# Kernel tuning notes

Measured on AMD Instinct MI355X. Metric: run time of the kernel, lower is better.

The kernel has to match this reference:

```python
import jax, jax.numpy as jnp
import numpy as np

OUT_H, OUT_W = 7, 7
SCALE = 0.25
S = 2  # sample_num per bin axis


def _bilinear(img, y, x):
    """Bilinearly sample img[..., H, W] at float coords (y, x).
    y, x have identical shape G; returns img.shape[:-2] + G.
    Matches RoIAlign CUDA interpolation (zero outside [-1, H]/[-1, W])."""
    H, W = img.shape[-2], img.shape[-1]
    valid = (y > -1.0) & (y < H) & (x > -1.0) & (x < W)
    y = jnp.clip(y, 0.0, H - 1)
    x = jnp.clip(x, 0.0, W - 1)
    y0 = jnp.floor(y).astype(jnp.int32)
    x0 = jnp.floor(x).astype(jnp.int32)
    y1 = jnp.minimum(y0 + 1, H - 1)
    x1 = jnp.minimum(x0 + 1, W - 1)
    ly = y - y0
    lx = x - x0
    hy, hx = 1.0 - ly, 1.0 - lx
    v = (hy * hx * img[..., y0, x0] + hy * lx * img[..., y0, x1]
         + ly * hx * img[..., y1, x0] + ly * lx * img[..., y1, x1])
    return jnp.where(valid, v, 0.0)


def setup_inputs() -> dict:
    key = jax.random.key(0)
    k1, k2, k3, k4, k5 = jax.random.split(key, 5)
    N, C, H, W = 2, 256, 200, 200
    R, MH, MW = 512, 128, 128
    features = jax.random.normal(k1, (N, C, H, W), jnp.float32)
    bidx = jax.random.randint(k2, (R,), 0, N)
    xy1 = jax.random.randint(k3, (R, 2), 0, 672)          # x1, y1 (image coords)
    wh = jax.random.randint(k4, (R, 2), 8, 128)           # box sizes in [8,128)
    xy2 = jnp.minimum(xy1 + wh - 1, 799)                  # x2, y2 inclusive
    rois = jnp.concatenate([bidx[:, None].astype(jnp.float32),
                            xy1.astype(jnp.float32),
                            xy2.astype(jnp.float32)], axis=1)  # [R,5]
    batch_masks = jax.random.uniform(k5, (R, MH, MW), jnp.float32)
    # zero-pad beyond each roi's (h, w), mimicking the list->dense packing
    hv = jnp.arange(MH)[None, :] < (xy2[:, 1] - xy1[:, 1] + 1)[:, None]
    wv = jnp.arange(MW)[None, :] < (xy2[:, 0] - xy1[:, 0] + 1)[:, None]
    batch_masks = batch_masks * (hv[:, :, None] & wv[:, None, :]).astype(jnp.float32)
    return {"features": features, "rois": rois, "batch_masks": batch_masks}


def reference(features, rois, batch_masks):
    """Mask-weighted RoIAlign: per-roi bilinear feature samples are weighted by
    the roi's shape mask (bilinearly sampled in roi-relative image coords),
    then average-pooled over the sub-sample grid of each output bin."""
    C = features.shape[1]

    def one_roi(roi, mask):
        b = roi[0].astype(jnp.int32)
        x1, y1, x2, y2 = roi[1], roi[2], roi[3], roi[4]
        roi_start_w = x1 * SCALE
        roi_start_h = y1 * SCALE
        roi_w = jnp.maximum((x2 - x1 + 1.0) * SCALE, 1.0)
        roi_h = jnp.maximum((y2 - y1 + 1.0) * SCALE, 1.0)
        bin_w = roi_w / OUT_W
        bin_h = roi_h / OUT_H
        # sub-sample offsets: (bin + (i+0.5)/S) for i in [0,S)  -> [OUT*S]
        offs = (jnp.arange(S, dtype=jnp.float32) + 0.5) / S
        ys = roi_start_h + (jnp.arange(OUT_H, dtype=jnp.float32)[:, None] + offs[None, :]).reshape(-1) * bin_h
        xs = roi_start_w + (jnp.arange(OUT_W, dtype=jnp.float32)[:, None] + offs[None, :]).reshape(-1) * bin_w
        yy, xx = jnp.meshgrid(ys, xs, indexing='ij')       # [OUT_H*S, OUT_W*S]
        feat = features[b]                                  # [C, H, W]
        vals = _bilinear(feat, yy, xx)                      # [C, OUT_H*S, OUT_W*S]
        # mask weight at the same sample point, in roi-relative image coords
        my = jnp.clip(yy / SCALE - y1, 0.0, y2 - y1)
        mx = jnp.clip(xx / SCALE - x1, 0.0, x2 - x1)
        wgt = _bilinear(mask, my, mx)                       # [OUT_H*S, OUT_W*S]
        v = (vals * wgt).reshape(C, OUT_H, S, OUT_W, S)
        return v.mean(axis=(2, 4))                          # [C, OUT_H, OUT_W]

    return jax.vmap(one_roi)(rois, batch_masks)             # [R, C, OUT_H, OUT_W]
```

## Files before the change

### kernel.cpp

```cpp
#include <hip/hip_runtime.h>


constexpr int   OUT_H = 7, OUT_W = 7;
constexpr int   NBIN  = OUT_H * OUT_W;
constexpr float SCALE = 0.25f;
constexpr int   S     = 2;
constexpr int   NSAMP = NBIN * S * S;
constexpr int   CG    = 8;
constexpr int   NPAIR = CG / 2;
constexpr int   RDIM  = 34;
constexpr int   RCOLS = 40;
constexpr int   NPIX  = RDIM * RCOLS;
constexpr int   PSTRIDE = NPIX * 2 + 4;

typedef unsigned short ushort_t;

__device__ __forceinline__ ushort_t f2bf(float f) {
    unsigned u = __float_as_uint(f);
    u += 0x7fffu + ((u >> 16) & 1u);
    return (ushort_t)(u >> 16);
}

__global__ __launch_bounds__(256, 6)
void roialign_direct_kernel(const float* __restrict__ features,
                            const float* __restrict__ rois,
                            const float* __restrict__ masks,
                            float*       __restrict__ out,
                            int C, int H, int W, int MH, int MW) {
    __shared__ __align__(16) ushort_t s_reg[NPAIR * PSTRIDE];
    __shared__ ushort4 s_idx[NSAMP];
    __shared__ float4  s_w[NSAMP];

    const int r   = blockIdx.x;
    const int cg  = blockIdx.y;
    const int tid = threadIdx.x;

    const float* roi = rois + (size_t)r * 5;
    const int   b  = (int)roi[0];
    const float x1 = roi[1], y1 = roi[2], x2 = roi[3], y2 = roi[4];

    const float roi_start_w = x1 * SCALE;
    const float roi_start_h = y1 * SCALE;
    const float roi_w = fmaxf((x2 - x1 + 1.0f) * SCALE, 1.0f);
    const float roi_h = fmaxf((y2 - y1 + 1.0f) * SCALE, 1.0f);
    const float bin_w = roi_w * (1.0f / OUT_W);
    const float bin_h = roi_h * (1.0f / OUT_H);

    int y_lo = (int)floorf(roi_start_h); y_lo = max(0, min(y_lo, H - 1));
    int x_lo = (int)floorf(roi_start_w); x_lo = max(0, min(x_lo, W - 1));
    const int y_hi = max(y_lo, min((int)floorf(roi_start_h + roi_h) + 1, H - 1));
    const int x_hi = max(x_lo, min((int)floorf(roi_start_w + roi_w) + 1, W - 1));
    const int rows  = min(y_hi - y_lo + 1, RDIM);
    const int x_lo4 = x_lo & ~3;
    const int cols4 = min((x_hi - x_lo4 + 4) >> 2, RCOLS / 4);

    {
        const int g    = tid >> 5;
        const int lane = tid & 31;
        const int pr   = g >> 1;
        const int part = g & 1;
        const size_t HWs = (size_t)H * W;
        const float* srcE = features + ((size_t)b * C + (size_t)(cg * CG + 2 * pr)) * HWs
                          + (size_t)y_lo * W + x_lo4;
        const float* srcO = srcE + HWs;
        unsigned* dp32base = (unsigned*)(s_reg + pr * PSTRIDE);
        const int items = rows * cols4;
        const float rcp = 1.0f / (float)cols4;
        for (int it = lane + part * 32; it < items; it += 64) {
            int ry = (int)((float)it * rcp);
            int k  = it - ry * cols4;
            if (k >= cols4) { ry++; k -= cols4; }
            if (k < 0)      { ry--; k += cols4; }
            const float4 vE = *(const float4*)(srcE + ry * W + 4 * k);
            const float4 vO = *(const float4*)(srcO + ry * W + 4 * k);
            const int pix = ry * RCOLS + 4 * k;
            uint2 a, c2;
            a.x  = (unsigned)f2bf(vE.x) | ((unsigned)f2bf(vO.x) << 16);
            a.y  = (unsigned)f2bf(vE.y) | ((unsigned)f2bf(vO.y) << 16);
            c2.x = (unsigned)f2bf(vE.z) | ((unsigned)f2bf(vO.z) << 16);
            c2.y = (unsigned)f2bf(vE.w) | ((unsigned)f2bf(vO.w) << 16);
            *(uint2*)(dp32base + pix)     = a;
            *(uint2*)(dp32base + pix + 2) = c2;
        }
    }

    if (tid < NSAMP) {
        const int bin = tid >> 2;
        const int sub = tid & 3;
        const int ph  = bin / OUT_W, pw = bin % OUT_W;
        const int iy  = sub >> 1,   ix = sub & 1;

        const float yy = roi_start_h + ((float)ph + ((float)iy + 0.5f) * (1.0f / S)) * bin_h;
        const float xx = roi_start_w + ((float)pw + ((float)ix + 0.5f) * (1.0f / S)) * bin_w;

        const bool valid = (yy > -1.0f) && (yy < (float)H) && (xx > -1.0f) && (xx < (float)W);

        const float* msk = masks + (size_t)r * MH * MW;
        float my = fminf(fmaxf(yy * (1.0f / SCALE) - y1, 0.0f), y2 - y1);
        float mx = fminf(fmaxf(xx * (1.0f / SCALE) - x1, 0.0f), x2 - x1);
        my = fminf(fmaxf(my, 0.0f), (float)(MH - 1));
        mx = fminf(fmaxf(mx, 0.0f), (float)(MW - 1));
        const int my0 = (int)floorf(my), mx0 = (int)floorf(mx);
        const int my1 = min(my0 + 1, MH - 1), mx1 = min(mx0 + 1, MW - 1);
        const float mly = my - (float)my0, mlx = mx - (float)mx0;
        const float mhy = 1.0f - mly,      mhx = 1.0f - mlx;
        const float wgt = mhy * mhx * msk[my0 * MW + mx0] + mhy * mlx * msk[my0 * MW + mx1]
                        + mly * mhx * msk[my1 * MW + mx0] + mly * mlx * msk[my1 * MW + mx1];

        const float yc = fminf(fmaxf(yy, 0.0f), (float)(H - 1));
        const float xc = fminf(fmaxf(xx, 0.0f), (float)(W - 1));
        const int y0  = (int)floorf(yc), x0 = (int)floorf(xc);
        const int y1i = min(y0 + 1, H - 1), x1i = min(x0 + 1, W - 1);
        const float ly = yc - (float)y0, lx = xc - (float)x0;
        const float hy = 1.0f - ly,      hx = 1.0f - lx;

        const int ly0 = min(max(y0  - y_lo,  0), RDIM  - 1);
        const int ly1 = min(max(y1i - y_lo,  0), RDIM  - 1);
        const int lx0 = min(max(x0  - x_lo4, 0), RCOLS - 1);
        const int lx1 = min(max(x1i - x_lo4, 0), RCOLS - 1);

        const float scale_all = (valid ? wgt : 0.0f) * (1.0f / (float)(S * S));
        ushort4 ix4;
        ix4.x = (ushort_t)((ly0 * RCOLS + lx0) * 4);
        ix4.y = (ushort_t)((ly0 * RCOLS + lx1) * 4);
        ix4.z = (ushort_t)((ly1 * RCOLS + lx0) * 4);
        ix4.w = (ushort_t)((ly1 * RCOLS + lx1) * 4);
        s_idx[tid] = ix4;
        float4 w4;
        w4.x = hy * hx * scale_all;
        w4.y = hy * lx * scale_all;
        w4.z = ly * hx * scale_all;
        w4.w = ly * lx * scale_all;
        s_w[tid] = w4;
    }
    __syncthreads();

    float accE = 0.0f, accO = 0.0f;
    const int pr  = tid & 3;
    const int bin = tid >> 2;
    if (tid < NSAMP) {
        const char* base = (const char*)s_reg + pr * (PSTRIDE * 2);
#pragma unroll
        for (int sub = 0; sub < 4; ++sub) {
            const int s = bin * 4 + sub;
            const ushort4 off = s_idx[s];
            const float4  w   = s_w[s];
            const unsigned q0 = *(const unsigned*)(base + off.x);
            const unsigned q1 = *(const unsigned*)(base + off.y);
            const unsigned q2 = *(const unsigned*)(base + off.z);
            const unsigned q3 = *(const unsigned*)(base + off.w);
            accE = fmaf(w.x, __uint_as_float(q0 << 16),          accE);
            accO = fmaf(w.x, __uint_as_float(q0 & 0xffff0000u),  accO);
            accE = fmaf(w.y, __uint_as_float(q1 << 16),          accE);
            accO = fmaf(w.y, __uint_as_float(q1 & 0xffff0000u),  accO);
            accE = fmaf(w.z, __uint_as_float(q2 << 16),          accE);
            accO = fmaf(w.z, __uint_as_float(q2 & 0xffff0000u),  accO);
            accE = fmaf(w.w, __uint_as_float(q3 << 16),          accE);
            accO = fmaf(w.w, __uint_as_float(q3 & 0xffff0000u),  accO);
        }
    }
    __syncthreads();

    float* s_out = (float*)s_reg;
    if (tid < NSAMP) {
        s_out[(2 * pr + 0) * NBIN + bin] = accE;
        s_out[(2 * pr + 1) * NBIN + bin] = accO;
    }
    __syncthreads();

    float* outr = out + ((size_t)r * C + (size_t)cg * CG) * NBIN;
    for (int i = tid; i < CG * NBIN; i += 256)
        outr[i] = s_out[i];
}

__global__ __launch_bounds__(256)
void mask_roialign_kernel(const float* __restrict__ features,
                          const float* __restrict__ rois,
                          const float* __restrict__ masks,
                          float*       __restrict__ out,
                          int C, int H, int W, int MH, int MW) {
    int blk = blockIdx.x;
    int pw  = blk % OUT_W;
    int ph  = (blk / OUT_W) % OUT_H;
    int r   = blk / (OUT_W * OUT_H);
    int c   = threadIdx.x;
    if (c >= C) return;

    const float* roi = rois + (size_t)r * 5;
    int   b  = (int)roi[0];
    float x1 = roi[1], y1 = roi[2], x2 = roi[3], y2 = roi[4];

    float roi_start_w = x1 * SCALE;
    float roi_start_h = y1 * SCALE;
    float roi_w = fmaxf((x2 - x1 + 1.0f) * SCALE, 1.0f);
    float roi_h = fmaxf((y2 - y1 + 1.0f) * SCALE, 1.0f);
    float bin_w = roi_w / (float)OUT_W;
    float bin_h = roi_h / (float)OUT_H;

    const float* fch = features + ((size_t)b * C + c) * (size_t)(H * W);
    const float* msk = masks + (size_t)r * MH * MW;

    float acc = 0.0f;
#pragma unroll
    for (int iy = 0; iy < S; ++iy) {
        float yy = roi_start_h + ((float)ph + ((float)iy + 0.5f) / (float)S) * bin_h;
#pragma unroll
        for (int ix = 0; ix < S; ++ix) {
            float xx = roi_start_w + ((float)pw + ((float)ix + 0.5f) / (float)S) * bin_w;
            bool valid = (yy > -1.0f) && (yy < (float)H) && (xx > -1.0f) && (xx < (float)W);
            float my = fminf(fmaxf(yy / SCALE - y1, 0.0f), fminf(y2 - y1, (float)(MH - 1)));
            float mx = fminf(fmaxf(xx / SCALE - x1, 0.0f), fminf(x2 - x1, (float)(MW - 1)));
            int my0 = (int)floorf(my), mx0 = (int)floorf(mx);
            int my1 = min(my0 + 1, MH - 1), mx1 = min(mx0 + 1, MW - 1);
            float mly = my - my0, mlx = mx - mx0, mhy = 1.0f - mly, mhx = 1.0f - mlx;
            float wgt = mhy * mhx * msk[my0 * MW + mx0] + mhy * mlx * msk[my0 * MW + mx1]
                      + mly * mhx * msk[my1 * MW + mx0] + mly * mlx * msk[my1 * MW + mx1];
            if (valid) {
                float yc = fminf(fmaxf(yy, 0.0f), (float)(H - 1));
                float xc = fminf(fmaxf(xx, 0.0f), (float)(W - 1));
                int y0 = (int)floorf(yc), x0 = (int)floorf(xc);
                int y1i = min(y0 + 1, H - 1), x1i = min(x0 + 1, W - 1);
                float ly = yc - y0, lx = xc - x0, hy = 1.0f - ly, hx = 1.0f - lx;
                float v = hy * hx * fch[y0  * W + x0 ] + hy * lx * fch[y0  * W + x1i]
                        + ly * hx * fch[y1i * W + x0 ] + ly * lx * fch[y1i * W + x1i];
                acc += wgt * v;
            }
        }
    }
    out[((size_t)r * C + c) * (size_t)NBIN + ph * OUT_W + pw] = acc * (1.0f / (S * S));
}

extern "C" void kernel_launch(void* const* d_in, const int* in_sizes, int n_in,
                              void* d_out, int out_size, void* d_ws, size_t ws_size,
                              hipStream_t stream) {
    const float* features = (const float*)d_in[0];
    const float* rois     = (const float*)d_in[1];
    const float* masks    = (const float*)d_in[2];
    float*       out      = (float*)d_out;

    const int R  = in_sizes[1] / 5;
    const int C  = out_size / (R * NBIN);
    const int H  = 200, W = 200;
    const int MH = 128, MW = 128;

    (void)d_ws; (void)ws_size;

    if ((C % CG == 0) && (W % 4 == 0)) {
        roialign_direct_kernel<<<dim3(R, C / CG), dim3(256), 0, stream>>>(
            features, rois, masks, out, C, H, W, MH, MW);
    } else {
        mask_roialign_kernel<<<dim3(R * NBIN), dim3(256), 0, stream>>>(
            features, rois, masks, out, C, H, W, MH, MW);
    }
}
```

Before: 179.1 us.

## Swap grid order to group ROIs, hoist mask loads, use bf16 pair conversion

Swaps the grid so consecutive blocks share one ROI and walk over channel groups instead of walking over ROIs for a fixed channel group, which changes L2 reuse of the ROI's feature window and mask rows. Mask gathers are issued before the feature staging loop so their latency overlaps with it. The hand-written bf16 rounding is replaced with the library float2-to-bfloat162 conversion, and the staging loop is unrolled by two. Consecutive blocks now read different channel planes of the same spatial region, so L2 locality could get better or worse.

```diff
diff --git a/kernel.cpp b/kernel.cpp
--- a/kernel.cpp
+++ b/kernel.cpp
@@ -1,4 +1,5 @@
 #include <hip/hip_runtime.h>
+#include <hip/hip_bf16.h>
 
 
 constexpr int   OUT_H = 7, OUT_W = 7;
@@ -10,15 +11,15 @@
 constexpr int   NPAIR = CG / 2;
 constexpr int   RDIM  = 34;
 constexpr int   RCOLS = 40;
-constexpr int   NPIX  = RDIM * RCOLS;
-constexpr int   PSTRIDE = NPIX * 2 + 4;
+constexpr int   PSTRIDE = RDIM * RCOLS * 2 + 4;
 
 typedef unsigned short ushort_t;
 
-__device__ __forceinline__ ushort_t f2bf(float f) {
-    unsigned u = __float_as_uint(f);
-    u += 0x7fffu + ((u >> 16) & 1u);
-    return (ushort_t)(u >> 16);
+__device__ __forceinline__ unsigned pack_bf16_pair(float e, float o) {
+    __hip_bfloat162 h2 = __float22bfloat162_rn(make_float2(e, o));
+    unsigned u;
+    __builtin_memcpy(&u, &h2, sizeof(u));
+    return u;
 }
 
 __global__ __launch_bounds__(256, 6)
@@ -31,8 +32,8 @@
     __shared__ ushort4 s_idx[NSAMP];
     __shared__ float4  s_w[NSAMP];
 
-    const int r   = blockIdx.x;
-    const int cg  = blockIdx.y;
+    const int cgp = blockIdx.x;
+    const int r   = blockIdx.y;
     const int tid = threadIdx.x;
 
     const float* roi = rois + (size_t)r * 5;
@@ -54,18 +55,43 @@
     const int x_lo4 = x_lo & ~3;
     const int cols4 = min((x_hi - x_lo4 + 4) >> 2, RCOLS / 4);
 
+    float yy = 0.f, xx = 0.f, m00 = 0.f, m01 = 0.f, m10 = 0.f, m11 = 0.f;
+    float mly = 0.f, mlx = 0.f;
+    if (tid < NSAMP) {
+        const int bin = tid >> 2;
+        const int sub = tid & 3;
+        const int ph  = bin / OUT_W, pw = bin % OUT_W;
+        const int iy  = sub >> 1,   ix = sub & 1;
+        yy = roi_start_h + ((float)ph + ((float)iy + 0.5f) * (1.0f / S)) * bin_h;
+        xx = roi_start_w + ((float)pw + ((float)ix + 0.5f) * (1.0f / S)) * bin_w;
+
+        const float* msk = masks + (size_t)r * MH * MW;
+        float my = fminf(fmaxf(yy * (1.0f / SCALE) - y1, 0.0f), y2 - y1);
+        float mx = fminf(fmaxf(xx * (1.0f / SCALE) - x1, 0.0f), x2 - x1);
+        my = fminf(fmaxf(my, 0.0f), (float)(MH - 1));
+        mx = fminf(fmaxf(mx, 0.0f), (float)(MW - 1));
+        const int my0 = (int)floorf(my), mx0 = (int)floorf(mx);
+        const int my1 = min(my0 + 1, MH - 1), mx1 = min(mx0 + 1, MW - 1);
+        mly = my - (float)my0; mlx = mx - (float)mx0;
+        m00 = msk[my0 * MW + mx0];
+        m01 = msk[my0 * MW + mx1];
+        m10 = msk[my1 * MW + mx0];
+        m11 = msk[my1 * MW + mx1];
+    }
+
     {
         const int g    = tid >> 5;
         const int lane = tid & 31;
         const int pr   = g >> 1;
         const int part = g & 1;
         const size_t HWs = (size_t)H * W;
-        const float* srcE = features + ((size_t)b * C + (size_t)(cg * CG + 2 * pr)) * HWs
+        const float* srcE = features + ((size_t)b * C + (size_t)(cgp * CG + 2 * pr)) * HWs
                           + (size_t)y_lo * W + x_lo4;
         const float* srcO = srcE + HWs;
         unsigned* dp32base = (unsigned*)(s_reg + pr * PSTRIDE);
         const int items = rows * cols4;
         const float rcp = 1.0f / (float)cols4;
+#pragma unroll 2
         for (int it = lane + part * 32; it < items; it += 64) {
             int ry = (int)((float)it * rcp);
             int k  = it - ry * cols4;
@@ -75,37 +101,20 @@
             const float4 vO = *(const float4*)(srcO + ry * W + 4 * k);
             const int pix = ry * RCOLS + 4 * k;
             uint2 a, c2;
-            a.x  = (unsigned)f2bf(vE.x) | ((unsigned)f2bf(vO.x) << 16);
-            a.y  = (unsigned)f2bf(vE.y) | ((unsigned)f2bf(vO.y) << 16);
-            c2.x = (unsigned)f2bf(vE.z) | ((unsigned)f2bf(vO.z) << 16);
-            c2.y = (unsigned)f2bf(vE.w) | ((unsigned)f2bf(vO.w) << 16);
+            a.x  = pack_bf16_pair(vE.x, vO.x);
+            a.y  = pack_bf16_pair(vE.y, vO.y);
+            c2.x = pack_bf16_pair(vE.z, vO.z);
+            c2.y = pack_bf16_pair(vE.w, vO.w);
             *(uint2*)(dp32base + pix)     = a;
             *(uint2*)(dp32base + pix + 2) = c2;
         }
     }
 
     if (tid < NSAMP) {
-        const int bin = tid >> 2;
-        const int sub = tid & 3;
-        const int ph  = bin / OUT_W, pw = bin % OUT_W;
-        const int iy  = sub >> 1,   ix = sub & 1;
-
-        const float yy = roi_start_h + ((float)ph + ((float)iy + 0.5f) * (1.0f / S)) * bin_h;
-        const float xx = roi_start_w + ((float)pw + ((float)ix + 0.5f) * (1.0f / S)) * bin_w;
-
         const bool valid = (yy > -1.0f) && (yy < (float)H) && (xx > -1.0f) && (xx < (float)W);
-
-        const float* msk = masks + (size_t)r * MH * MW;
-        float my = fminf(fmaxf(yy * (1.0f / SCALE) - y1, 0.0f), y2 - y1);
-        float mx = fminf(fmaxf(xx * (1.0f / SCALE) - x1, 0.0f), x2 - x1);
-        my = fminf(fmaxf(my, 0.0f), (float)(MH - 1));
-        mx = fminf(fmaxf(mx, 0.0f), (float)(MW - 1));
-        const int my0 = (int)floorf(my), mx0 = (int)floorf(mx);
-        const int my1 = min(my0 + 1, MH - 1), mx1 = min(mx0 + 1, MW - 1);
-        const float mly = my - (float)my0, mlx = mx - (float)mx0;
-        const float mhy = 1.0f - mly,      mhx = 1.0f - mlx;
-        const float wgt = mhy * mhx * msk[my0 * MW + mx0] + mhy * mlx * msk[my0 * MW + mx1]
-                        + mly * mhx * msk[my1 * MW + mx0] + mly * mlx * msk[my1 * MW + mx1];
+        const float mhy = 1.0f - mly, mhx = 1.0f - mlx;
+        const float wgt = mhy * mhx * m00 + mhy * mlx * m01
+                        + mly * mhx * m10 + mly * mlx * m11;
 
         const float yc = fminf(fmaxf(yy, 0.0f), (float)(H - 1));
         const float xc = fminf(fmaxf(xx, 0.0f), (float)(W - 1));
@@ -120,12 +129,12 @@
         const int lx1 = min(max(x1i - x_lo4, 0), RCOLS - 1);
 
         const float scale_all = (valid ? wgt : 0.0f) * (1.0f / (float)(S * S));
-        ushort4 ix4;
-        ix4.x = (ushort_t)((ly0 * RCOLS + lx0) * 4);
-        ix4.y = (ushort_t)((ly0 * RCOLS + lx1) * 4);
-        ix4.z = (ushort_t)((ly1 * RCOLS + lx0) * 4);
-        ix4.w = (ushort_t)((ly1 * RCOLS + lx1) * 4);
-        s_idx[tid] = ix4;
+        ushort4 o;
+        o.x = (ushort_t)((ly0 * RCOLS + lx0) * 4);
+        o.y = (ushort_t)((ly0 * RCOLS + lx1) * 4);
+        o.z = (ushort_t)((ly1 * RCOLS + lx0) * 4);
+        o.w = (ushort_t)((ly1 * RCOLS + lx1) * 4);
+        s_idx[tid] = o;
         float4 w4;
         w4.x = hy * hx * scale_all;
         w4.y = hy * lx * scale_all;
@@ -168,7 +177,7 @@
     }
     __syncthreads();
 
-    float* outr = out + ((size_t)r * C + (size_t)cg * CG) * NBIN;
+    float* outr = out + ((size_t)r * C + (size_t)cgp * CG) * NBIN;
     for (int i = tid; i < CG * NBIN; i += 256)
         outr[i] = s_out[i];
 }
@@ -246,7 +255,7 @@
     (void)d_ws; (void)ws_size;
 
     if ((C % CG == 0) && (W % 4 == 0)) {
-        roialign_direct_kernel<<<dim3(R, C / CG), dim3(256), 0, stream>>>(
+        roialign_direct_kernel<<<dim3(C / CG, R), dim3(256), 0, stream>>>(
             features, rois, masks, out, C, H, W, MH, MW);
     } else {
         mask_roialign_kernel<<<dim3(R * NBIN), dim3(256), 0, stream>>>(
```

After: 180.7 us. About the same (+0.9%).
